# Kernel tuning notes

Measured on AMD Instinct MI355X. Metric: run time of the kernel, lower is better.

## Reference

```python
import jax, jax.numpy as jnp
import numpy as np
import math

N, CDCT, HB, WB = 8, 64, 128, 128
E, NH, KSZ, DFF, NL = 128, 4, 7, 512, 4
P = KSZ * KSZ
EPS = 1e-5


def setup_inputs() -> dict:
    key = jax.random.key(0)
    ks = iter(jax.random.split(key, 40))
    f = lambda shape, s=0.05: jax.random.normal(next(ks), shape, jnp.float32) * s
    inp = {
        'dct': jax.random.normal(next(ks), (N, CDCT, HB, WB), jnp.float32),
        'qt': jax.random.uniform(next(ks), (N, CDCT), jnp.float32, 0.1, 2.0),
        # BlockEncoder (FiLM): conv1 3x3 (64->64), conv2 1x1 (64->128)
        'enc_c1_w': f((CDCT, CDCT, 3, 3)),
        'enc_c1_b': jnp.zeros((CDCT,), jnp.float32),
        'enc_c2_w': f((E, CDCT)),  # 1x1 conv as (out,in)
        'enc_c2_b': jnp.zeros((E,), jnp.float32),
        # per-layer stacked transformer params
        'ln1_g': jnp.ones((NL, E), jnp.float32),
        'ln1_b': jnp.zeros((NL, E), jnp.float32),
        'q_w': f((NL, E, E)), 'q_b': jnp.zeros((NL, E), jnp.float32),
        'k_w': f((NL, E, E)), 'k_b': jnp.zeros((NL, E), jnp.float32),
        'v_w': f((NL, E, E)), 'v_b': jnp.zeros((NL, E), jnp.float32),
        'rel_bias': f((NL, NH, P), 0.02),
        'ln2_g': jnp.ones((NL, E), jnp.float32),
        'ln2_b': jnp.zeros((NL, E), jnp.float32),
        'ff_w1': f((NL, E, DFF)), 'ff_b1': jnp.zeros((NL, DFF), jnp.float32),
        'ff_w2': f((NL, DFF, E)), 'ff_b2': jnp.zeros((NL, E), jnp.float32),
        # BlockDecoder (FiLM): 1x1 conv (128->64)
        'dec_w': f((CDCT, E)),
        'dec_b': jnp.zeros((CDCT,), jnp.float32),
    }
    return inp


def _ln(x, g, b):
    m = x.mean(-1, keepdims=True)
    v = ((x - m) ** 2).mean(-1, keepdims=True)
    return (x - m) / jnp.sqrt(v + EPS) * g + b


def _local_attn(y, qw, qb, kw, kb, vw, vb, rb):
    # y: (N,H,W,E). Sliding-window attention, window KSZ x KSZ, zero-padded.
    n, h, w, e = y.shape
    dk = e // NH
    pad = KSZ // 2
    q = (jnp.einsum('nhwi,io->nhwo', y, qw) + qb).reshape(n, h, w, NH, dk)
    k = jnp.einsum('nhwi,io->nhwo', y, kw) + kb
    v = jnp.einsum('nhwi,io->nhwo', y, vw) + vb
    kp = jnp.pad(k, ((0, 0), (pad, pad), (pad, pad), (0, 0)))
    vp = jnp.pad(v, ((0, 0), (pad, pad), (pad, pad), (0, 0)))
    scores = []
    for i in range(KSZ):  # fixed small window loop; avoids P-fold K/V blowup
        for j in range(KSZ):
            ks_ = kp[:, i:i + h, j:j + w, :].reshape(n, h, w, NH, dk)
            scores.append(jnp.einsum('nhwkd,nhwkd->nhwk', q, ks_))
    s = jnp.stack(scores, axis=-1) / math.sqrt(e) + rb  # (N,H,W,NH,P), rb (NH,P)
    a = jax.nn.softmax(s, axis=-1)
    out = jnp.zeros_like(q)
    idx = 0
    for i in range(KSZ):
        for j in range(KSZ):
            vs = vp[:, i:i + h, j:j + w, :].reshape(n, h, w, NH, dk)
            out = out + a[..., idx, None] * vs
            idx += 1
    return out.reshape(n, h, w, e)


def reference(dct, qt, enc_c1_w, enc_c1_b, enc_c2_w, enc_c2_b,
              ln1_g, ln1_b, q_w, q_b, k_w, k_b, v_w, v_b, rel_bias,
              ln2_g, ln2_b, ff_w1, ff_b1, ff_w2, ff_b2, dec_w, dec_b):
    # BlockEncoder (FiLM)
    c1 = jax.lax.conv_general_dilated(
        dct, enc_c1_w, (1, 1), 'SAME',
        dimension_numbers=('NCHW', 'OIHW', 'NCHW')) + enc_c1_b[None, :, None, None]
    film = qt[:, :, None, None] * c1
    emb = jnp.einsum('nihw,oi->nohw', dct + film, enc_c2_w) + enc_c2_b[None, :, None, None]
    x = emb.transpose(0, 2, 3, 1)  # (N,H,W,E)
    # SpectralTransformer
    for l in range(NL):
        y0 = _ln(x, ln1_g[l], ln1_b[l])
        y2 = _local_attn(y0, q_w[l], q_b[l], k_w[l], k_b[l], v_w[l], v_b[l], rel_bias[l])
        y3 = _ln(y2 + x, ln2_g[l], ln2_b[l])
        h = jax.nn.gelu(jnp.einsum('nhwi,io->nhwo', y3, ff_w1[l]) + ff_b1[l], approximate=False)
        x = y2 + jnp.einsum('nhwi,io->nhwo', h, ff_w2[l]) + ff_b2[l]
    # BlockDecoder (FiLM)
    res = (jnp.einsum('nhwi,oi->nohw', x, dec_w) + dec_b[None, :, None, None]) * qt[:, :, None, None]
    return dct + res
```

## Files before the change

### kernel.cpp

```cpp
#include <hip/hip_runtime.h>
#include <hip/hip_bf16.h>

typedef __attribute__((ext_vector_type(8))) short short8;
typedef __attribute__((ext_vector_type(4))) float floatx4;
typedef unsigned short u16;
typedef unsigned int u32;

#define T_TOK 131072
#define LN_EPS 1e-5f
#define ATTN_SCALE 0.08838834764831845f

__device__ __forceinline__ u16 f2b(float f){
  __hip_bfloat16 h = __float2bfloat16(f);
  return *reinterpret_cast<u16*>(&h);
}
__device__ __forceinline__ float blo(u32 u){ union{u32 i; float f;} c; c.i = u<<16; return c.f; }
__device__ __forceinline__ float bhi(u32 u){ union{u32 i; float f;} c; c.i = u & 0xffff0000u; return c.f; }
__device__ __forceinline__ u32 pk2(float lo, float hi){
  return (u32)f2b(lo) | ((u32)f2b(hi)<<16);
}

__global__ __launch_bounds__(256) void trans_k(
    const float* __restrict__ dct, u16* __restrict__ dctT)
{
  __shared__ u16 tl[256][66];
  int tid = threadIdx.x;
  int p = blockIdx.x*256 + tid;
  int n = p >> 14;
  int r = p & 16383;
  const float* dctn = dct + (long)n*64*16384;
  #pragma unroll
  for (int c=0;c<64;c++) tl[tid][c] = f2b(dctn[c*16384 + r]);
  __syncthreads();
  long base = (long)blockIdx.x*256*64;
  for (int pass=0; pass<64; pass++){
    int idx = pass*256 + tid;
    int pp = idx>>6, o = idx&63;
    dctT[base + idx] = tl[pp][o];
  }
}

__global__ __launch_bounds__(256) void convgemm_k(
    const u16* __restrict__ dctT, const uint4* __restrict__ cwB,
    const float* __restrict__ c1b, const float* __restrict__ qt,
    u16* __restrict__ tbuf)
{
  __shared__ uint4 AL[3120];
  int tid = threadIdx.x, wave = tid>>6, lane = tid&63;
  int l15 = lane & 15, quad = lane >> 4;
  int bm = blockIdx.x*128;
  int n = bm >> 14;
  int yb = (bm & 16383) >> 7;
  int wm = wave*32;
  for (int i = tid; i < 3120; i += 256){
    int row = i / 1040;
    int rem = i - row*1040;
    int pxs = rem >> 3;
    int k8 = rem & 7;
    int grow = yb + row - 1;
    int gpx = pxs - 1;
    uint4 v = {0,0,0,0};
    if (((unsigned)grow < 128u) && ((unsigned)gpx < 128u))
      v = *reinterpret_cast<const uint4*>(dctT + ((long)bm + (row-1)*128 + gpx)*64 + k8*8);
    AL[row*1040 + (pxs<<3) + (k8 ^ (pxs&7))] = v;
  }
  float qv[4], bi4[4];
  #pragma unroll
  for (int nt=0; nt<4; nt++){
    int col = nt*16 + l15;
    bi4[nt] = c1b[col];
    qv[nt] = qt[n*64 + col];
  }
  uint4 bcur[8];
  #pragma unroll
  for (int i=0;i<8;i++) bcur[i] = cwB[i*64 + lane];

  floatx4 acc[2][4];
  #pragma unroll
  for (int i=0;i<2;i++)
    #pragma unroll
    for (int j=0;j<4;j++)
      #pragma unroll
      for (int e=0;e<4;e++) acc[i][j][e]=0.f;

  __syncthreads();

  #pragma unroll
  for (int tap=0; tap<9; tap++){
    int dy = tap/3 - 1, dx = tap%3 - 1;
    uint4 bnx[8];
    if (tap < 8){
      #pragma unroll
      for (int i=0;i<8;i++) bnx[i] = cwB[(tap+1)*512 + i*64 + lane];
    }
    short8 af[2][2];
    #pragma unroll
    for (int mt=0; mt<2; mt++)
      #pragma unroll
      for (int ks=0; ks<2; ks++){
        int pxs = wm + mt*16 + l15 + dx + 1;
        int k8 = ks*4 + quad;
        af[mt][ks] = *reinterpret_cast<const short8*>(
            &AL[(dy+1)*1040 + (pxs<<3) + (k8 ^ (pxs&7))]);
      }
    #pragma unroll
    for (int ks=0; ks<2; ks++)
      #pragma unroll
      for (int mt=0; mt<2; mt++)
        #pragma unroll
        for (int nt=0; nt<4; nt++)
          acc[mt][nt] = __builtin_amdgcn_mfma_f32_16x16x32_bf16(
              af[mt][ks],
              *reinterpret_cast<const short8*>(&bcur[nt*2+ks]),
              acc[mt][nt], 0,0,0);
    #pragma unroll
    for (int i=0;i<8;i++) bcur[i] = bnx[i];
  }
  const u16* ALu = (const u16*)AL;
  #pragma unroll
  for (int mt=0; mt<2; mt++){
    #pragma unroll
    for (int nt=0; nt<4; nt++){
      int col = nt*16 + l15;
      int k8c = col>>3, sub = col&7;
      #pragma unroll
      for (int rr2=0; rr2<4; rr2++){
        int p = wm + mt*16 + quad*4 + rr2;
        int pxs = p + 1;
        float cen = blo((u32)ALu[(((130 + pxs)<<3) + (k8c ^ (pxs&7)))*8 + sub]);
        float val = acc[mt][nt][rr2] + bi4[nt];
        tbuf[((long)bm + p)*64 + col] = f2b(cen + qv[nt]*val);
      }
    }
  }
}

__global__ __launch_bounds__(256) void prep_k(
    const float* __restrict__ qw, const float* __restrict__ kw,
    const float* __restrict__ vw, const float* __restrict__ qb2,
    const float* __restrict__ kb2, const float* __restrict__ vb2,
    const float* __restrict__ f1, const float* __restrict__ f2,
    const float* __restrict__ c1w,
    u16* __restrict__ qkvB, u16* __restrict__ ff1B,
    u16* __restrict__ ff2B, float* __restrict__ biasB,
    uint4* __restrict__ cwB)
{
  int idx = blockIdx.x*256 + threadIdx.x;
  if (idx < 196608){
    int l = idx / 49152, r = idx % 49152;
    int sel = r / 16384, rr = r % 16384;
    int k = rr >> 7, nn = rr & 127;
    const float* src = (sel==0? qw : sel==1? kw : vw) + l*16384 + rr;
    qkvB[(size_t)l*49152 + (size_t)(sel*128 + nn)*128 + k] = f2b(*src);
  } else if (idx < 458752){
    int e = idx - 196608; int l = e >> 16, r = e & 65535;
    int k = r >> 9, nn = r & 511;
    ff1B[(size_t)l*65536 + (size_t)nn*128 + k] = f2b(f1[(size_t)l*65536 + r]);
  } else if (idx < 720896){
    int e = idx - 458752; int l = e >> 16, r = e & 65535;
    int k = r >> 7, nn = r & 127;
    ff2B[(size_t)l*65536 + (size_t)nn*512 + k] = f2b(f2[(size_t)l*65536 + r]);
  } else if (idx < 722432){
    int e = idx - 720896;
    int l = e / 384, c = e % 384;
    int sel = c >> 7, nn = c & 127;
    const float* src = (sel==0? qb2 : sel==1? kb2 : vb2) + l*128 + nn;
    biasB[e] = *src;
  } else if (idx < 727040){
    int e = idx - 722432;
    int s = e & 511;
    int tap = e >> 9;
    int fn = s>>7, rr = s&127, fk2 = rr>>6, t = rr&63, q = t>>4, nr = t&15;
    int nn = fn*16+nr, k8 = fk2*4+q;
    const float* wp = c1w + nn*576 + k8*72 + tap;
    uint4 pk;
    pk.x = (u32)f2b(wp[0])  | ((u32)f2b(wp[9]) <<16);
    pk.y = (u32)f2b(wp[18]) | ((u32)f2b(wp[27])<<16);
    pk.z = (u32)f2b(wp[36]) | ((u32)f2b(wp[45])<<16);
    pk.w = (u32)f2b(wp[54]) | ((u32)f2b(wp[63])<<16);
    cwB[e] = pk;
  }
}

__global__ __launch_bounds__(256) void stats_k(
    const float* __restrict__ x, const u16* __restrict__ yb,
    float* __restrict__ st)
{
  int wave = threadIdx.x>>6, lane = threadIdx.x&63;
  long t = (long)blockIdx.x*4 + wave;
  long idx = t*128 + lane*2;
  float2 vv = *reinterpret_cast<const float2*>(x+idx);
  if (yb){
    u32 p = *reinterpret_cast<const u32*>(yb+idx);
    vv.x += blo(p); vv.y += bhi(p);
  }
  float s = vv.x+vv.y, sq = vv.x*vv.x + vv.y*vv.y;
  #pragma unroll
  for (int o2=32;o2;o2>>=1){ s += __shfl_xor(s,o2); sq += __shfl_xor(sq,o2); }
  float mean = s*(1.f/128.f);
  float var = sq*(1.f/128.f) - mean*mean;
  if (lane==0){
    float2 ms; ms.x = mean; ms.y = rsqrtf(var + LN_EPS);
    *reinterpret_cast<float2*>(st + t*2) = ms;
  }
}

__global__ __launch_bounds__(256,2) void qkv_k(
    const float* __restrict__ x, const float* __restrict__ st,
    const float* __restrict__ lng, const float* __restrict__ lnb,
    const u16* __restrict__ B16, const float* __restrict__ bias,
    u16* __restrict__ qkv)
{
  __shared__ uint4 As[2048];
  int tid = threadIdx.x, wave = tid>>6, lane = tid&63;
  int l15 = lane&15, quad = lane>>4;
  int bm = blockIdx.x*128;
  int wm = (wave>>1)*64, wn = (wave&1)*64;
  int wmf = wm>>4;
  #pragma unroll
  for (int pS=0; pS<8; pS++){
    int s = pS*256 + tid;
    int kh = s>>10, rem = s&1023;
    int fm = rem>>7, rr = rem&127, fk2 = rr>>6, t = rr&63, q2 = t>>4, mr = t&15;
    int m = fm*16+mr;
    int kk = kh*64 + (fk2*4+q2)*8;
    long row = bm + m;
    const float* xp = x + row*128 + kk;
    float4 a = *reinterpret_cast<const float4*>(xp);
    float4 b4 = *reinterpret_cast<const float4*>(xp+4);
    float v[8] = {a.x,a.y,a.z,a.w,b4.x,b4.y,b4.z,b4.w};
    float2 ms = *reinterpret_cast<const float2*>(st + row*2);
    #pragma unroll
    for (int j=0;j<8;j++) v[j] = (v[j]-ms.x)*ms.y*lng[kk+j] + lnb[kk+j];
    uint4 pk;
    pk.x = pk2(v[0],v[1]); pk.y = pk2(v[2],v[3]);
    pk.z = pk2(v[4],v[5]); pk.w = pk2(v[6],v[7]);
    As[s] = pk;
  }
  __syncthreads();
  #pragma unroll 1
  for (int nb=0; nb<3; nb++){
    floatx4 acc[4][4];
    #pragma unroll
    for (int i=0;i<4;i++)
      #pragma unroll
      for (int j=0;j<4;j++)
        #pragma unroll
        for (int e=0;e<4;e++) acc[i][j][e]=0.f;
    #pragma unroll
    for (int kh=0; kh<2; kh++)
      #pragma unroll
      for (int ks=0; ks<2; ks++){
        short8 af[4], bf[4];
        #pragma unroll
        for (int mt=0; mt<4; mt++)
          af[mt] = *reinterpret_cast<const short8*>(&As[kh*1024 + ((wmf+mt)*2+ks)*64 + lane]);
        #pragma unroll
        for (int nt=0; nt<4; nt++)
          bf[nt] = *reinterpret_cast<const short8*>(
              B16 + (nb*128 + wn + nt*16 + l15)*128 + kh*64 + (ks*4+quad)*8);
        #pragma unroll
        for (int mt=0;mt<4;mt++)
          #pragma unroll
          for (int nt=0;nt<4;nt++)
            acc[mt][nt] = __builtin_amdgcn_mfma_f32_16x16x32_bf16(af[mt], bf[nt], acc[mt][nt], 0,0,0);
      }
    #pragma unroll
    for (int nt=0;nt<4;nt++){
      int col = nb*128 + wn + nt*16 + l15;
      float bi = bias[col];
      #pragma unroll
      for (int mt=0;mt<4;mt++){
        int row0 = bm + wm + mt*16 + quad*4;
        #pragma unroll
        for (int r=0;r<4;r++)
          qkv[(long)(row0+r)*384 + col] = f2b(acc[mt][nt][r] + bi);
      }
    }
  }
}

__global__ __launch_bounds__(256,2) void ff_k(
    const float* __restrict__ x, const u16* __restrict__ y2b,
    const float* __restrict__ st,
    const float* __restrict__ lng, const float* __restrict__ lnb,
    const u16* __restrict__ w1, const u16* __restrict__ w2,
    const float* __restrict__ b1, const float* __restrict__ b2,
    float* __restrict__ xo)
{
  __shared__ uint4 As[2048];
  __shared__ u16 Hs[16384];
  int tid = threadIdx.x, wave = tid>>6, lane = tid&63;
  int l15 = lane&15, quad = lane>>4;
  int bm = blockIdx.x*128;
  int wm = (wave>>1)*64, wn = (wave&1)*64;
  int wmf = wm>>4;
  #pragma unroll
  for (int pS=0; pS<8; pS++){
    int s = pS*256 + tid;
    int kh = s>>10, rem = s&1023;
    int fm = rem>>7, rr = rem&127, fk2 = rr>>6, t = rr&63, q2 = t>>4, mr = t&15;
    int m = fm*16+mr;
    int kk = kh*64 + (fk2*4+q2)*8;
    long row = bm + m;
    const float* xp = x + row*128 + kk;
    float4 a = *reinterpret_cast<const float4*>(xp);
    float4 b4 = *reinterpret_cast<const float4*>(xp+4);
    float v[8] = {a.x,a.y,a.z,a.w,b4.x,b4.y,b4.z,b4.w};
    uint4 yv = *reinterpret_cast<const uint4*>(y2b + row*128 + kk);
    v[0]+=blo(yv.x); v[1]+=bhi(yv.x); v[2]+=blo(yv.y); v[3]+=bhi(yv.y);
    v[4]+=blo(yv.z); v[5]+=bhi(yv.z); v[6]+=blo(yv.w); v[7]+=bhi(yv.w);
    float2 ms = *reinterpret_cast<const float2*>(st + row*2);
    #pragma unroll
    for (int j=0;j<8;j++) v[j] = (v[j]-ms.x)*ms.y*lng[kk+j] + lnb[kk+j];
    uint4 pk;
    pk.x = pk2(v[0],v[1]); pk.y = pk2(v[2],v[3]);
    pk.z = pk2(v[4],v[5]); pk.w = pk2(v[6],v[7]);
    As[s] = pk;
  }
  __syncthreads();

  floatx4 acc2[4][4];
  #pragma unroll
  for (int i=0;i<4;i++)
    #pragma unroll
    for (int j=0;j<4;j++)
      #pragma unroll
      for (int e=0;e<4;e++) acc2[i][j][e]=0.f;

  #pragma unroll 1
  for (int kc=0; kc<4; kc++){
    floatx4 acc1[4][4];
    #pragma unroll
    for (int i=0;i<4;i++)
      #pragma unroll
      for (int j=0;j<4;j++)
        #pragma unroll
        for (int e=0;e<4;e++) acc1[i][j][e]=0.f;
    #pragma unroll
    for (int kh=0; kh<2; kh++)
      #pragma unroll
      for (int ks=0; ks<2; ks++){
        short8 af[4], bf[4];
        #pragma unroll
        for (int mt=0; mt<4; mt++)
          af[mt] = *reinterpret_cast<const short8*>(&As[kh*1024 + ((wmf+mt)*2+ks)*64 + lane]);
        #pragma unroll
        for (int nt=0; nt<4; nt++)
          bf[nt] = *reinterpret_cast<const short8*>(
              w1 + (kc*128 + wn + nt*16 + l15)*128 + kh*64 + (ks*4+quad)*8);
        #pragma unroll
        for (int mt=0;mt<4;mt++)
          #pragma unroll
          for (int nt=0;nt<4;nt++)
            acc1[mt][nt] = __builtin_amdgcn_mfma_f32_16x16x32_bf16(af[mt], bf[nt], acc1[mt][nt], 0,0,0);
      }
    float b1v[4];
    #pragma unroll
    for (int nt=0;nt<4;nt++) b1v[nt] = b1[kc*128 + wn + nt*16 + l15];
    #pragma unroll
    for (int mt=0;mt<4;mt++)
      #pragma unroll
      for (int nt=0;nt<4;nt++){
        int col = wn + nt*16 + l15;
        int c8 = col>>3, c7 = col&7;
        #pragma unroll
        for (int r=0;r<4;r++){
          int row = wm + mt*16 + quad*4 + r;
          float val = acc1[mt][nt][r] + b1v[nt];
          float g = 0.5f*val*(1.f + erff(val*0.70710678118654752f));
          Hs[(row<<7) + ((c8 ^ (row&7))<<3) + c7] = f2b(g);
        }
      }
    __syncthreads();
    #pragma unroll
    for (int kh=0; kh<2; kh++)
      #pragma unroll
      for (int ks=0; ks<2; ks++){
        short8 af[4], bf[4];
        #pragma unroll
        for (int mt=0;mt<4;mt++){
          int row = wm + mt*16 + l15;
          int col8 = kh*8 + ks*4 + quad;
          af[mt] = *reinterpret_cast<const short8*>(
              &Hs[(row<<7) + ((col8 ^ (row&7))<<3)]);
        }
        #pragma unroll
        for (int nt=0;nt<4;nt++)
          bf[nt] = *reinterpret_cast<const short8*>(
              w2 + (wn + nt*16 + l15)*512 + kc*128 + kh*64 + (ks*4+quad)*8);
        #pragma unroll
        for (int mt=0;mt<4;mt++)
          #pragma unroll
          for (int nt=0;nt<4;nt++)
            acc2[mt][nt] = __builtin_amdgcn_mfma_f32_16x16x32_bf16(af[mt], bf[nt], acc2[mt][nt], 0,0,0);
      }
    if (kc < 3) __syncthreads();
  }
  #pragma unroll
  for (int nt=0;nt<4;nt++){
    int col = wn + nt*16 + l15;
    float bi = b2[col];
    #pragma unroll
    for (int mt=0;mt<4;mt++){
      int row0 = bm + wm + mt*16 + quad*4;
      #pragma unroll
      for (int r=0;r<4;r++){
        long row = row0 + r;
        xo[row*128 + col] = acc2[mt][nt][r] + bi + blo((u32)y2b[row*128 + col]);
      }
    }
  }
}

constexpr int EPI_F32 = 0;
constexpr int EPI_DEC = 4;
constexpr int ASRC_B16 = 0;
constexpr int BSRC_F32 = 0;

template<int BN, int EPI, int ASRC, int BSRC>
__global__ __launch_bounds__(256) void gemm_k(
    const u16* __restrict__ A16, const float* __restrict__ Axf,
    const u16* __restrict__ Yadd, const float* __restrict__ st,
    const float* __restrict__ lng, const float* __restrict__ lnb,
    const float* __restrict__ Bsrc, const u16* __restrict__ B16,
    const float* __restrict__ bias, const u16* __restrict__ resid,
    float* __restrict__ outF, u16* __restrict__ outB,
    int M, int N, int K, int bNK,
    const float* __restrict__ qtp, const float* __restrict__ dctp)
{
  static_assert(BN==128 || BN==64, "BN");
  constexpr int MF = (BN==128)?4:2;
  constexpr int BSLOT = (BN/16)*128;
  __shared__ uint4 As[1024];
  __shared__ uint4 Bs[BSLOT];
  int tid = threadIdx.x;
  int wave = tid>>6, lane = tid&63;
  int bm = blockIdx.x * 128;
  int bn = blockIdx.y * BN;
  int wm = (BN==128)? (wave>>1)*64 : wave*32;
  int wn = (BN==128)? (wave&1)*64 : 0;
  int wmf = wm>>4, wnf = wn>>4;
  floatx4 acc[MF][4];
  #pragma unroll
  for (int i=0;i<MF;i++)
    #pragma unroll
    for (int j=0;j<4;j++)
      #pragma unroll
      for (int e=0;e<4;e++) acc[i][j][e]=0.f;

  for (int k0=0; k0<K; k0+=64){
    __syncthreads();
    #pragma unroll
    for (int pS=0; pS<4; pS++){
      int s = pS*256 + tid;
      int fm = s>>7, rr = s&127, fk2 = rr>>6, t = rr&63, quad = t>>4, mr = t&15;
      int m = fm*16+mr, k8 = fk2*4+quad;
      int kk = k0 + k8*8;
      long row = bm + m;
      As[s] = *reinterpret_cast<const uint4*>(A16 + row*K + kk);
    }
    #pragma unroll
    for (int pS=0; pS<BSLOT/256; pS++){
      int s = pS*256 + tid;
      int fn = s>>7, rr = s&127, fk2 = rr>>6, t = rr&63, quad = t>>4, nr = t&15;
      int nn = fn*16+nr, k8 = fk2*4+quad;
      int kk = k0 + k8*8;
      float v[8];
      if (bNK){
        const float* src = Bsrc + (long)(bn+nn)*K + kk;
        float4 a = *reinterpret_cast<const float4*>(src);
        float4 b = *reinterpret_cast<const float4*>(src+4);
        v[0]=a.x; v[1]=a.y; v[2]=a.z; v[3]=a.w; v[4]=b.x; v[5]=b.y; v[6]=b.z; v[7]=b.w;
      } else {
        #pragma unroll
        for (int j=0;j<8;j++) v[j] = Bsrc[(long)(kk+j)*N + bn + nn];
      }
      uint4 pk;
      pk.x = pk2(v[0],v[1]); pk.y = pk2(v[2],v[3]);
      pk.z = pk2(v[4],v[5]); pk.w = pk2(v[6],v[7]);
      Bs[s] = pk;
    }
    __syncthreads();
    #pragma unroll
    for (int ks=0; ks<2; ks++){
      short8 af[MF], bfr[4];
      #pragma unroll
      for (int mt=0; mt<MF; mt++)
        af[mt] = *reinterpret_cast<const short8*>(&As[((wmf+mt)*2+ks)*64 + lane]);
      #pragma unroll
      for (int nt=0; nt<4; nt++)
        bfr[nt] = *reinterpret_cast<const short8*>(&Bs[((wnf+nt)*2+ks)*64 + lane]);
      #pragma unroll
      for (int mt=0; mt<MF; mt++)
        #pragma unroll
        for (int nt=0; nt<4; nt++)
          acc[mt][nt] = __builtin_amdgcn_mfma_f32_16x16x32_bf16(af[mt], bfr[nt], acc[mt][nt], 0,0,0);
    }
  }
  #pragma unroll
  for (int mt=0; mt<MF; mt++){
    #pragma unroll
    for (int nt=0; nt<4; nt++){
      int col = bn + wn + nt*16 + (lane&15);
      int row0 = bm + wm + mt*16 + ((lane>>4)<<2);
      float bi = bias[col];
      #pragma unroll
      for (int rr2=0; rr2<4; rr2++){
        long row = row0 + rr2;
        float val = acc[mt][nt][rr2] + bi;
        if constexpr (EPI==EPI_F32){
          outF[row*N + col] = val;
        } else {
          int nn2 = (int)(row>>14), rm = (int)(row&16383);
          long didx = ((long)(nn2*64 + col)<<14) + rm;
          outF[didx] = dctp[didx] + val*qtp[nn2*64+col];
        }
      }
    }
  }
}

__global__ __launch_bounds__(256) void attn_k(
    const u16* __restrict__ qkv, const float* __restrict__ rb,
    u16* __restrict__ y2b)
{
  __shared__ __align__(16) char lds_all[4*7168];
  int tid = threadIdx.x, wave = tid>>6, lane = tid&63;
  int l15 = lane & 15, quad = lane >> 4;
  char* wl = lds_all + wave*7168;
  u16* Kl = (u16*)wl;
  u16* Vt = (u16*)(wl + 2560);
  float* ebl = (float*)(wl + 5120);
  int bi = blockIdx.x;
  int n = bi >> 8, t2 = bi & 255;
  int ty = (t2 >> 4) << 3, tx = (t2 & 15) << 3;
  int hh = wave;
  for (int k = lane; k < 512; k += 64){
    int dyp = k / 21, dxp = k - dyp*21;
    int dy = dyp - 7, dx = dxp - 7;
    float v = 0.f;
    if (((unsigned)dy < 7u) && ((unsigned)dx < 7u))
      v = __expf(rb[hh*49 + dy*7 + dx]);
    ebl[k] = v;
  }
  short8 qf[4];
  #pragma unroll
  for (int mt=0; mt<4; mt++){
    int m = mt*16 + l15;
    long tq = (long)n*16384 + (long)(ty + (m>>3))*128 + (tx + (m&7));
    qf[mt] = *reinterpret_cast<const short8*>(qkv + tq*384 + hh*32 + quad*8);
  }
  int pxs[2], c8s[2];
  #pragma unroll
  for (int ps=0; ps<2; ps++){
    int s = ps*64 + lane;
    pxs[ps] = s >> 2; c8s[ps] = s & 3;
  }
  auto load_chunk = [&](int c, uint4* krr, uint4* vrr){
    #pragma unroll
    for (int ps=0; ps<2; ps++){
      int hp = c*32 + pxs[ps];
      int hy = hp / 14, hx = hp % 14;
      int gy = ty + hy - 3, gx = tx + hx - 3;
      uint4 kz = {0,0,0,0}, vz = {0,0,0,0};
      if (((unsigned)gy < 128u) && ((unsigned)gx < 128u)){
        long t = (long)n*16384 + gy*128 + gx;
        const u16* p = qkv + t*384 + hh*32 + c8s[ps]*8;
        kz = *reinterpret_cast<const uint4*>(p + 128);
        vz = *reinterpret_cast<const uint4*>(p + 256);
      }
      krr[ps] = kz; vrr[ps] = vz;
    }
  };
  uint4 kr[2], vr[2];
  load_chunk(0, kr, vr);

  floatx4 oacc[4][2];
  float lsum[4];
  #pragma unroll
  for (int mt=0;mt<4;mt++){
    lsum[mt] = 0.f;
    #pragma unroll
    for (int nf=0;nf<2;nf++)
      #pragma unroll
      for (int e=0;e<4;e++) oacc[mt][nf][e]=0.f;
  }
  int qb0 = (l15>>3)*21 + (l15&7);
  bool lower = (lane < 32);
  bool sendRecv = (quad==0) || (quad==3);
  bool qodd = (quad & 1) != 0;
  bool q0q = (quad==0), q1q = (quad==1);

  for (int c=0; c<7; c++){
    #pragma unroll
    for (int ps=0; ps<2; ps++){
      *reinterpret_cast<uint4*>(Kl + pxs[ps]*40 + c8s[ps]*8) = kr[ps];
      u32 wv[4] = {vr[ps].x, vr[ps].y, vr[ps].z, vr[ps].w};
      #pragma unroll
      for (int i=0;i<8;i++){
        u16 val = (u16)((wv[i>>1] >> ((i&1)*16)) & 0xffffu);
        Vt[(c8s[ps]*8 + i)*40 + pxs[ps]] = val;
      }
    }
    uint4 kr2[2], vr2[2];
    if (c < 6) load_chunk(c+1, kr2, vr2);
    short8 kf0 = *reinterpret_cast<const short8*>(Kl + l15*40 + quad*8);
    short8 kf1 = *reinterpret_cast<const short8*>(Kl + (16 + l15)*40 + quad*8);
    short8 vf0 = *reinterpret_cast<const short8*>(Vt + l15*40 + quad*8);
    short8 vf1 = *reinterpret_cast<const short8*>(Vt + (16 + l15)*40 + quad*8);
    int hb[2][4];
    #pragma unroll
    for (int nf=0;nf<2;nf++)
      #pragma unroll
      for (int r=0;r<4;r++){
        int hp = c*32 + nf*16 + quad*4 + r;
        int hy = hp / 14, hx = hp - hy*14;
        hb[nf][r] = hy*21 + hx + 154;
      }
    #pragma unroll
    for (int mt=0;mt<4;mt++){
      floatx4 zz; zz[0]=0.f; zz[1]=0.f; zz[2]=0.f; zz[3]=0.f;
      floatx4 s0 = __builtin_amdgcn_mfma_f32_16x16x32_bf16(kf0, qf[mt], zz, 0,0,0);
      floatx4 s1 = __builtin_amdgcn_mfma_f32_16x16x32_bf16(kf1, qf[mt], zz, 0,0,0);
      int qb = qb0 + mt*42;
      float p0[4], p1[4];
      #pragma unroll
      for (int r=0;r<4;r++){
        p0[r] = __expf(s0[r]*ATTN_SCALE) * ebl[hb[0][r] - qb];
        p1[r] = __expf(s1[r]*ATTN_SCALE) * ebl[hb[1][r] - qb];
      }
      lsum[mt] += ((p0[0]+p0[1]) + (p0[2]+p0[3])) + ((p1[0]+p1[1]) + (p1[2]+p1[3]));
      u32 Aw = pk2(p0[0], p0[1]);
      u32 Bw = pk2(p0[2], p0[3]);
      u32 Cw = pk2(p1[0], p1[1]);
      u32 Dw = pk2(p1[2], p1[3]);
      u32 own0 = lower ? Aw : Cw;
      u32 own1 = lower ? Bw : Dw;
      u32 recv1 = (u32)__shfl_xor((int)(lower ? Cw : Aw), 32);
      u32 recv2 = (u32)__shfl_xor((int)(lower ? Dw : Bw), 32);
      u32 r3 = (u32)__shfl_xor((int)(sendRecv ? recv1 : own0), 16);
      u32 r4 = (u32)__shfl_xor((int)(sendRecv ? recv2 : own1), 16);
      uint4 paw;
      paw.x = qodd ? r3 : (q0q ? own0 : recv1);
      paw.y = qodd ? r4 : (q0q ? own1 : recv2);
      paw.z = qodd ? (q1q ? recv1 : own0) : r3;
      paw.w = qodd ? (q1q ? recv2 : own1) : r4;
      short8 pa = *reinterpret_cast<const short8*>(&paw);
      oacc[mt][0] = __builtin_amdgcn_mfma_f32_16x16x32_bf16(pa, vf0, oacc[mt][0], 0,0,0);
      oacc[mt][1] = __builtin_amdgcn_mfma_f32_16x16x32_bf16(pa, vf1, oacc[mt][1], 0,0,0);
    }
    #pragma unroll
    for (int ps=0; ps<2; ps++){ kr[ps]=kr2[ps]; vr[ps]=vr2[ps]; }
  }
  float rinv[4];
  #pragma unroll
  for (int mt=0;mt<4;mt++){
    float s = lsum[mt];
    s += __shfl_xor(s, 16);
    s += __shfl_xor(s, 32);
    rinv[mt] = 1.0f / s;
  }
  #pragma unroll
  for (int mt=0;mt<4;mt++){
    #pragma unroll
    for (int r=0;r<4;r++){
      int row = mt*16 + quad*4 + r;
      float sc = __shfl(rinv[mt], (quad<<2) | r);
      long t = (long)n*16384 + (long)(ty + (row>>3))*128 + (tx + (row&7));
      #pragma unroll
      for (int nfv=0;nfv<2;nfv++)
        y2b[t*128 + hh*32 + nfv*16 + l15] = f2b(oacc[mt][nfv][r] * sc);
    }
  }
}

__global__ __launch_bounds__(256) void cvt_k(const float* __restrict__ x, u16* __restrict__ o){
  long i = ((long)blockIdx.x*256 + threadIdx.x)*4;
  float4 vv = *reinterpret_cast<const float4*>(x+i);
  uint2 pk;
  pk.x = (u32)f2b(vv.x) | ((u32)f2b(vv.y)<<16);
  pk.y = (u32)f2b(vv.z) | ((u32)f2b(vv.w)<<16);
  *reinterpret_cast<uint2*>(o+i) = pk;
}

extern "C" void kernel_launch(void* const* d_in, const int* in_sizes, int n_in,
                              void* d_out, int out_size, void* d_ws, size_t ws_size,
                              hipStream_t stream)
{
  (void)in_sizes; (void)n_in; (void)out_size; (void)ws_size;
  const float* dct  = (const float*)d_in[0];
  const float* qt   = (const float*)d_in[1];
  const float* c1w  = (const float*)d_in[2];
  const float* c1b  = (const float*)d_in[3];
  const float* c2w  = (const float*)d_in[4];
  const float* c2b  = (const float*)d_in[5];
  const float* ln1g = (const float*)d_in[6];
  const float* ln1b = (const float*)d_in[7];
  const float* qw   = (const float*)d_in[8];
  const float* qbv  = (const float*)d_in[9];
  const float* kw   = (const float*)d_in[10];
  const float* kbv  = (const float*)d_in[11];
  const float* vw   = (const float*)d_in[12];
  const float* vbv  = (const float*)d_in[13];
  const float* rel  = (const float*)d_in[14];
  const float* ln2g = (const float*)d_in[15];
  const float* ln2b = (const float*)d_in[16];
  const float* ffw1 = (const float*)d_in[17];
  const float* ffb1 = (const float*)d_in[18];
  const float* ffw2 = (const float*)d_in[19];
  const float* ffb2 = (const float*)d_in[20];
  const float* decw = (const float*)d_in[21];
  const float* decb = (const float*)d_in[22];
  float* out = (float*)d_out;

  char* w = (char*)d_ws;
  float* x    = (float*)w;
  float* st   = (float*)(w + 67108864);
  u16*  qkv   = (u16*)(w + 68157440);
  u16*  y2b   = (u16*)(w + 168820736);
  u16*  qkvB  = (u16*)(w + 202375168);
  u16*  ff1B  = (u16*)(w + 202768384);
  u16*  ff2B  = (u16*)(w + 203292672);
  float* biasB= (float*)(w + 203816960);
  uint4* cwB  = (uint4*)(w + 203823104);
  u16*  tbuf = y2b;
  u16*  dctT = qkv;
  u16*  xb   = y2b;

  prep_k<<<2840,256,0,stream>>>(qw,kw,vw,qbv,kbv,vbv,ffw1,ffw2,c1w,
                                qkvB,ff1B,ff2B,biasB,cwB);
  trans_k<<<512,256,0,stream>>>(dct, dctT);
  convgemm_k<<<1024,256,0,stream>>>(dctT, cwB, c1b, qt, tbuf);
  gemm_k<128,EPI_F32,ASRC_B16,BSRC_F32><<<dim3(1024,1),256,0,stream>>>(
      tbuf, nullptr,nullptr,nullptr,nullptr,nullptr,
      c2w, nullptr, c2b, nullptr, x, nullptr, T_TOK,128,64, 1, nullptr,nullptr);

  for (int l=0;l<4;l++){
    stats_k<<<32768,256,0,stream>>>(x, nullptr, st);
    qkv_k<<<1024,256,0,stream>>>(x, st, ln1g+l*128, ln1b+l*128,
        qkvB + (size_t)l*49152, biasB + l*384, qkv);
    attn_k<<<2048,256,0,stream>>>(qkv, rel+l*196, y2b);
    stats_k<<<32768,256,0,stream>>>(x, y2b, st);
    ff_k<<<1024,256,0,stream>>>(x, y2b, st, ln2g+l*128, ln2b+l*128,
        ff1B + (size_t)l*65536, ff2B + (size_t)l*65536,
        ffb1 + l*512, ffb2 + l*128, x);
  }
  cvt_k<<<16384,256,0,stream>>>(x, xb);
  gemm_k<64,EPI_DEC,ASRC_B16,BSRC_F32><<<dim3(1024,1),256,0,stream>>>(
      xb, nullptr,nullptr,nullptr,nullptr,nullptr,
      decw, nullptr, decb, nullptr, out, nullptr, T_TOK,64,128, 1, qt, dct);
}
```

Measured before the change: 1.336 ms.

## Restructure FFN kernel to keep hidden activations in registers via lane shuffles

The fused FFN kernel now runs 8 waves per block, each owning 16 tokens across all 512 hidden units, in place of a 2x2 wave tiling. The first GEMM is computed transposed (weights as the A operand), and the GELU outputs are rearranged with cross-lane shuffles directly into the A-operand layout of the second GEMM. This removes the shared-memory hidden buffer and its block-wide barriers. In exchange, each wave reloads all of W1 and W2 from global or cache per 16 tokens, so weight traffic per token rises, and more lane-shuffle work is added.

```diff
diff --git a/kernel.cpp b/kernel.cpp
--- a/kernel.cpp
+++ b/kernel.cpp
@@ -280,7 +280,7 @@
   }
 }
 
-__global__ __launch_bounds__(256,2) void ff_k(
+__global__ __launch_bounds__(512,2) void ff_k(
     const float* __restrict__ x, const u16* __restrict__ y2b,
     const float* __restrict__ st,
     const float* __restrict__ lng, const float* __restrict__ lnb,
@@ -289,15 +289,12 @@
     float* __restrict__ xo)
 {
   __shared__ uint4 As[2048];
-  __shared__ u16 Hs[16384];
   int tid = threadIdx.x, wave = tid>>6, lane = tid&63;
   int l15 = lane&15, quad = lane>>4;
   int bm = blockIdx.x*128;
-  int wm = (wave>>1)*64, wn = (wave&1)*64;
-  int wmf = wm>>4;
-  #pragma unroll
-  for (int pS=0; pS<8; pS++){
-    int s = pS*256 + tid;
+  #pragma unroll
+  for (int pS=0; pS<4; pS++){
+    int s = pS*512 + tid;
     int kh = s>>10, rem = s&1023;
     int fm = rem>>7, rr = rem&127, fk2 = rr>>6, t = rr&63, q2 = t>>4, mr = t&15;
     int m = fm*16+mr;
@@ -319,96 +316,80 @@
     As[s] = pk;
   }
   __syncthreads();
-
-  floatx4 acc2[4][4];
-  #pragma unroll
-  for (int i=0;i<4;i++)
-    #pragma unroll
-    for (int j=0;j<4;j++)
-      #pragma unroll
-      for (int e=0;e<4;e++) acc2[i][j][e]=0.f;
+  short8 atok[4];
+  #pragma unroll
+  for (int kh=0;kh<2;kh++)
+    #pragma unroll
+    for (int ks=0;ks<2;ks++)
+      atok[kh*2+ks] = *reinterpret_cast<const short8*>(
+          &As[kh*1024 + (wave*2+ks)*64 + lane]);
+
+  floatx4 acc2[8];
+  #pragma unroll
+  for (int i=0;i<8;i++)
+    #pragma unroll
+    for (int e=0;e<4;e++) acc2[i][e]=0.f;
+
+  bool lower = (lane < 32);
+  bool sendRecv = (quad==0) || (quad==3);
+  bool qodd = (quad & 1) != 0;
+  bool q0q = (quad==0), q1q = (quad==1);
 
   #pragma unroll 1
-  for (int kc=0; kc<4; kc++){
-    floatx4 acc1[4][4];
-    #pragma unroll
-    for (int i=0;i<4;i++)
-      #pragma unroll
-      for (int j=0;j<4;j++)
-        #pragma unroll
-        for (int e=0;e<4;e++) acc1[i][j][e]=0.f;
+  for (int c=0; c<16; c++){
+    floatx4 a0, a1;
+    #pragma unroll
+    for (int e=0;e<4;e++){ a0[e]=0.f; a1[e]=0.f; }
     #pragma unroll
     for (int kh=0; kh<2; kh++)
       #pragma unroll
       for (int ks=0; ks<2; ks++){
-        short8 af[4], bf[4];
-        #pragma unroll
-        for (int mt=0; mt<4; mt++)
-          af[mt] = *reinterpret_cast<const short8*>(&As[kh*1024 + ((wmf+mt)*2+ks)*64 + lane]);
-        #pragma unroll
-        for (int nt=0; nt<4; nt++)
-          bf[nt] = *reinterpret_cast<const short8*>(
-              w1 + (kc*128 + wn + nt*16 + l15)*128 + kh*64 + (ks*4+quad)*8);
-        #pragma unroll
-        for (int mt=0;mt<4;mt++)
-          #pragma unroll
-          for (int nt=0;nt<4;nt++)
-            acc1[mt][nt] = __builtin_amdgcn_mfma_f32_16x16x32_bf16(af[mt], bf[nt], acc1[mt][nt], 0,0,0);
-      }
-    float b1v[4];
-    #pragma unroll
-    for (int nt=0;nt<4;nt++) b1v[nt] = b1[kc*128 + wn + nt*16 + l15];
-    #pragma unroll
-    for (int mt=0;mt<4;mt++)
-      #pragma unroll
-      for (int nt=0;nt<4;nt++){
-        int col = wn + nt*16 + l15;
-        int c8 = col>>3, c7 = col&7;
-        #pragma unroll
-        for (int r=0;r<4;r++){
-          int row = wm + mt*16 + quad*4 + r;
-          float val = acc1[mt][nt][r] + b1v[nt];
-          float g = 0.5f*val*(1.f + erff(val*0.70710678118654752f));
-          Hs[(row<<7) + ((c8 ^ (row&7))<<3) + c7] = f2b(g);
-        }
-      }
-    __syncthreads();
-    #pragma unroll
-    for (int kh=0; kh<2; kh++)
-      #pragma unroll
-      for (int ks=0; ks<2; ks++){
-        short8 af[4], bf[4];
-        #pragma unroll
-        for (int mt=0;mt<4;mt++){
-          int row = wm + mt*16 + l15;
-          int col8 = kh*8 + ks*4 + quad;
-          af[mt] = *reinterpret_cast<const short8*>(
-              &Hs[(row<<7) + ((col8 ^ (row&7))<<3)]);
-        }
-        #pragma unroll
-        for (int nt=0;nt<4;nt++)
-          bf[nt] = *reinterpret_cast<const short8*>(
-              w2 + (wn + nt*16 + l15)*512 + kc*128 + kh*64 + (ks*4+quad)*8);
-        #pragma unroll
-        for (int mt=0;mt<4;mt++)
-          #pragma unroll
-          for (int nt=0;nt<4;nt++)
-            acc2[mt][nt] = __builtin_amdgcn_mfma_f32_16x16x32_bf16(af[mt], bf[nt], acc2[mt][nt], 0,0,0);
-      }
-    if (kc < 3) __syncthreads();
-  }
-  #pragma unroll
-  for (int nt=0;nt<4;nt++){
-    int col = wn + nt*16 + l15;
+        short8 w1f0 = *reinterpret_cast<const short8*>(
+            w1 + (c*32 + l15)*128 + kh*64 + ks*32 + quad*8);
+        short8 w1f1 = *reinterpret_cast<const short8*>(
+            w1 + (c*32 + 16 + l15)*128 + kh*64 + ks*32 + quad*8);
+        a0 = __builtin_amdgcn_mfma_f32_16x16x32_bf16(w1f0, atok[kh*2+ks], a0, 0,0,0);
+        a1 = __builtin_amdgcn_mfma_f32_16x16x32_bf16(w1f1, atok[kh*2+ks], a1, 0,0,0);
+      }
+    float g0[4], g1[4];
+    #pragma unroll
+    for (int r=0;r<4;r++){
+      float v0 = a0[r] + b1[c*32 + quad*4 + r];
+      float v1 = a1[r] + b1[c*32 + 16 + quad*4 + r];
+      g0[r] = 0.5f*v0*(1.f + erff(v0*0.70710678118654752f));
+      g1[r] = 0.5f*v1*(1.f + erff(v1*0.70710678118654752f));
+    }
+    u32 Aw = pk2(g0[0], g0[1]);
+    u32 Bw = pk2(g0[2], g0[3]);
+    u32 Cw = pk2(g1[0], g1[1]);
+    u32 Dw = pk2(g1[2], g1[3]);
+    u32 own0 = lower ? Aw : Cw;
+    u32 own1 = lower ? Bw : Dw;
+    u32 recv1 = (u32)__shfl_xor((int)(lower ? Cw : Aw), 32);
+    u32 recv2 = (u32)__shfl_xor((int)(lower ? Dw : Bw), 32);
+    u32 r3 = (u32)__shfl_xor((int)(sendRecv ? recv1 : own0), 16);
+    u32 r4 = (u32)__shfl_xor((int)(sendRecv ? recv2 : own1), 16);
+    uint4 paw;
+    paw.x = qodd ? r3 : (q0q ? own0 : recv1);
+    paw.y = qodd ? r4 : (q0q ? own1 : recv2);
+    paw.z = qodd ? (q1q ? recv1 : own0) : r3;
+    paw.w = qodd ? (q1q ? recv2 : own1) : r4;
+    short8 pa = *reinterpret_cast<const short8*>(&paw);
+    #pragma unroll
+    for (int nt=0; nt<8; nt++){
+      short8 w2f = *reinterpret_cast<const short8*>(
+          w2 + (nt*16 + l15)*512 + c*32 + quad*8);
+      acc2[nt] = __builtin_amdgcn_mfma_f32_16x16x32_bf16(pa, w2f, acc2[nt], 0,0,0);
+    }
+  }
+  #pragma unroll
+  for (int nt=0; nt<8; nt++){
+    int col = nt*16 + l15;
     float bi = b2[col];
     #pragma unroll
-    for (int mt=0;mt<4;mt++){
-      int row0 = bm + wm + mt*16 + quad*4;
-      #pragma unroll
-      for (int r=0;r<4;r++){
-        long row = row0 + r;
-        xo[row*128 + col] = acc2[mt][nt][r] + bi + blo((u32)y2b[row*128 + col]);
-      }
+    for (int r=0;r<4;r++){
+      long row = bm + wave*16 + quad*4 + r;
+      xo[row*128 + col] = acc2[nt][r] + bi + blo((u32)y2b[row*128 + col]);
     }
   }
 }
@@ -742,7 +723,7 @@
         qkvB + (size_t)l*49152, biasB + l*384, qkv);
     attn_k<<<2048,256,0,stream>>>(qkv, rel+l*196, y2b);
     stats_k<<<32768,256,0,stream>>>(x, y2b, st);
-    ff_k<<<1024,256,0,stream>>>(x, y2b, st, ln2g+l*128, ln2b+l*128,
+    ff_k<<<1024,512,0,stream>>>(x, y2b, st, ln2g+l*128, ln2b+l*128,
         ff1B + (size_t)l*65536, ff2B + (size_t)l*65536,
         ffb1 + l*512, ffb2 + l*128, x);
   }
```

Result: slower. 1.864 ms (+39.5%).

## Software-pipeline FFN hidden chunks with double-buffered GELU tile in LDS

Applied to the files above, without the earlier changes.

The fused FFN kernel now processes the hidden dimension in eight 64-wide chunks instead of four 128-wide ones. It double-buffers the GELU output in shared memory so the GEMM1 for chunk hc+1 is issued before GEMM2 of chunk hc. The goal is to overlap the MFMA work of the two GEMMs and the erf-heavy GELU, leaving one barrier per chunk instead of two. The cost is more loop iterations and barriers, and GEMM1 tiles shrink to 4x2, which lowers reuse of the w1 fragments.

```diff
diff --git a/kernel.cpp b/kernel.cpp
--- a/kernel.cpp
+++ b/kernel.cpp
@@ -289,11 +289,13 @@
     float* __restrict__ xo)
 {
   __shared__ uint4 As[2048];
-  __shared__ u16 Hs[16384];
+  __shared__ u16 Hs[2][8192];
   int tid = threadIdx.x, wave = tid>>6, lane = tid&63;
   int l15 = lane&15, quad = lane>>4;
   int bm = blockIdx.x*128;
-  int wm = (wave>>1)*64, wn = (wave&1)*64;
+  int wm = (wave>>1)*64;
+  int wn1 = (wave&1)*32;
+  int wn2 = (wave&1)*64;
   int wmf = wm>>4;
   #pragma unroll
   for (int pS=0; pS<8; pS++){
@@ -328,78 +330,95 @@
       #pragma unroll
       for (int e=0;e<4;e++) acc2[i][j][e]=0.f;
 
-  #pragma unroll 1
-  for (int kc=0; kc<4; kc++){
-    floatx4 acc1[4][4];
+  auto GEMM1 = [&](int hc, floatx4 (&acc1)[4][2]){
     #pragma unroll
     for (int i=0;i<4;i++)
       #pragma unroll
-      for (int j=0;j<4;j++)
+      for (int j=0;j<2;j++)
         #pragma unroll
         for (int e=0;e<4;e++) acc1[i][j][e]=0.f;
     #pragma unroll
     for (int kh=0; kh<2; kh++)
       #pragma unroll
       for (int ks=0; ks<2; ks++){
-        short8 af[4], bf[4];
+        short8 af[4], bf[2];
         #pragma unroll
         for (int mt=0; mt<4; mt++)
           af[mt] = *reinterpret_cast<const short8*>(&As[kh*1024 + ((wmf+mt)*2+ks)*64 + lane]);
         #pragma unroll
-        for (int nt=0; nt<4; nt++)
+        for (int nt=0; nt<2; nt++)
           bf[nt] = *reinterpret_cast<const short8*>(
-              w1 + (kc*128 + wn + nt*16 + l15)*128 + kh*64 + (ks*4+quad)*8);
+              w1 + (hc*64 + wn1 + nt*16 + l15)*128 + kh*64 + (ks*4+quad)*8);
         #pragma unroll
         for (int mt=0;mt<4;mt++)
           #pragma unroll
-          for (int nt=0;nt<4;nt++)
+          for (int nt=0;nt<2;nt++)
             acc1[mt][nt] = __builtin_amdgcn_mfma_f32_16x16x32_bf16(af[mt], bf[nt], acc1[mt][nt], 0,0,0);
       }
-    float b1v[4];
-    #pragma unroll
-    for (int nt=0;nt<4;nt++) b1v[nt] = b1[kc*128 + wn + nt*16 + l15];
+  };
+  auto GELUW = [&](int hc, floatx4 (&acc1)[4][2]){
+    float b1v[2];
+    #pragma unroll
+    for (int nt=0;nt<2;nt++) b1v[nt] = b1[hc*64 + wn1 + nt*16 + l15];
+    u16* hb = Hs[hc&1];
     #pragma unroll
     for (int mt=0;mt<4;mt++)
       #pragma unroll
-      for (int nt=0;nt<4;nt++){
-        int col = wn + nt*16 + l15;
+      for (int nt=0;nt<2;nt++){
+        int col = wn1 + nt*16 + l15;
         int c8 = col>>3, c7 = col&7;
         #pragma unroll
         for (int r=0;r<4;r++){
           int row = wm + mt*16 + quad*4 + r;
           float val = acc1[mt][nt][r] + b1v[nt];
           float g = 0.5f*val*(1.f + erff(val*0.70710678118654752f));
-          Hs[(row<<7) + ((c8 ^ (row&7))<<3) + c7] = f2b(g);
+          hb[(row<<6) + ((c8 ^ (row&7))<<3) + c7] = f2b(g);
         }
       }
-    __syncthreads();
-    #pragma unroll
-    for (int kh=0; kh<2; kh++)
-      #pragma unroll
-      for (int ks=0; ks<2; ks++){
-        short8 af[4], bf[4];
-        #pragma unroll
-        for (int mt=0;mt<4;mt++){
-          int row = wm + mt*16 + l15;
-          int col8 = kh*8 + ks*4 + quad;
-          af[mt] = *reinterpret_cast<const short8*>(
-              &Hs[(row<<7) + ((col8 ^ (row&7))<<3)]);
-        }
+  };
+  auto GEMM2 = [&](int hc){
+    const u16* hb = Hs[hc&1];
+    #pragma unroll
+    for (int ks2=0; ks2<2; ks2++){
+      short8 af[4], bf[4];
+      #pragma unroll
+      for (int mt=0;mt<4;mt++){
+        int row = wm + mt*16 + l15;
+        int col8 = ks2*4 + quad;
+        af[mt] = *reinterpret_cast<const short8*>(
+            &hb[(row<<6) + ((col8 ^ (row&7))<<3)]);
+      }
+      #pragma unroll
+      for (int nt=0;nt<4;nt++)
+        bf[nt] = *reinterpret_cast<const short8*>(
+            w2 + (wn2 + nt*16 + l15)*512 + hc*64 + ks2*32 + quad*8);
+      #pragma unroll
+      for (int mt=0;mt<4;mt++)
         #pragma unroll
         for (int nt=0;nt<4;nt++)
-          bf[nt] = *reinterpret_cast<const short8*>(
-              w2 + (wn + nt*16 + l15)*512 + kc*128 + kh*64 + (ks*4+quad)*8);
-        #pragma unroll
-        for (int mt=0;mt<4;mt++)
-          #pragma unroll
-          for (int nt=0;nt<4;nt++)
-            acc2[mt][nt] = __builtin_amdgcn_mfma_f32_16x16x32_bf16(af[mt], bf[nt], acc2[mt][nt], 0,0,0);
-      }
-    if (kc < 3) __syncthreads();
+          acc2[mt][nt] = __builtin_amdgcn_mfma_f32_16x16x32_bf16(af[mt], bf[nt], acc2[mt][nt], 0,0,0);
+    }
+  };
+
+  {
+    floatx4 acc1a[4][2];
+    GEMM1(0, acc1a);
+    GELUW(0, acc1a);
+  }
+  __syncthreads();
+  #pragma unroll 1
+  for (int hc=0; hc<8; hc++){
+    floatx4 acc1n[4][2];
+    if (hc < 7) GEMM1(hc+1, acc1n);
+    GEMM2(hc);
+    if (hc < 7){
+      GELUW(hc+1, acc1n);
+      __syncthreads();
+    }
   }
   #pragma unroll
   for (int nt=0;nt<4;nt++){
-    int col = wn + nt*16 + l15;
+    int col = wn2 + nt*16 + l15;
     float bi = b2[col];
     #pragma unroll
     for (int mt=0;mt<4;mt++){
```

Measured after the change: 1.343 ms. No clear change (+0.5%).
